# Kernel optimization log

Hardware: AMD Instinct MI355X
Metric: run time of the kernel (lower is better)

## Reference

```python
import jax, jax.numpy as jnp
import numpy as np

H = 8  # num_heads

def setup_inputs() -> dict:
    key = jax.random.key(0)
    k1, k2, k3, k4 = jax.random.split(key, 4)
    B, T, D, K = 16, 8192, 512, 4
    x = jax.random.normal(k1, (B, T, D), dtype=jnp.float32)
    mask = jax.random.randint(k2, (B, T), 0, 2, dtype=jnp.int32)
    queries = jax.random.normal(k3, (1, K, D), dtype=jnp.float32) * 0.02
    # xavier_uniform for (D, D) Linear weight
    limit = np.sqrt(6.0 / (D + D))
    w_out = jax.random.uniform(k4, (D, D), dtype=jnp.float32, minval=-limit, maxval=limit)
    b_out = jnp.zeros((D,), dtype=jnp.float32)
    return {"x": x, "mask": mask, "queries": queries, "w_out": w_out, "b_out": b_out}

def reference(x, mask, queries, w_out, b_out):
    B, T, D = x.shape
    K = queries.shape[1]
    hd = D // H
    scale = jnp.sqrt(jnp.float32(hd))
    q = queries.reshape(K, H, hd)          # shared across batch
    kv = x.reshape(B, T, H, hd)            # keys == values
    scores = jnp.einsum('khd,bthd->bhkt', q, kv) / scale  # (B,H,K,T)
    scores = jnp.where(mask[:, None, None, :] == 0, jnp.float32(-1e9), scores)
    attn = jax.nn.softmax(scores, axis=-1)  # dropout is identity in eval / p=0
    out = jnp.einsum('bhkt,bthd->bkhd', attn, kv).reshape(B, K, D)
    return out @ w_out.T + b_out
```

## Files before the change

### kernel.cpp

```cpp
#include <hip/hip_runtime.h>
#include <math.h>

#define BB 16
#define TT 8192
#define DD 512
#define KK 4
#define HH 8
#define HD 64

__global__ __launch_bounds__(512, 4)
void attn_partial_kernel(const float* __restrict__ x,
                         const int* __restrict__ mask,
                         const float* __restrict__ queries,
                         float* __restrict__ ws,
                         int NC) {
    const int C     = TT / NC;
    const int iters = C >> 3;
    const int b     = blockIdx.x / NC;
    const int c     = blockIdx.x % NC;
    const int t0    = c * C;
    const int tid   = threadIdx.x;
    const int slot  = tid >> 6;
    const int seg   = tid & 63;
    const int h     = seg >> 3;
    const int qd    = seg & 7;

    __shared__ int    smask[512];
    __shared__ float4 smerge[8 * 512];
    __shared__ float  smerge_l[8 * 32];

    for (int i = tid; i < C; i += 512) smask[i] = mask[b * TT + t0 + i];
    __syncthreads();

    const float4* q4 = reinterpret_cast<const float4*>(queries);
    float4 qv[4][2];
    #pragma unroll
    for (int k = 0; k < 4; ++k)
        #pragma unroll
        for (int j = 0; j < 2; ++j) {
            float4 v = q4[k * 128 + seg * 2 + j];
            v.x *= 0.125f; v.y *= 0.125f; v.z *= 0.125f; v.w *= 0.125f;
            qv[k][j] = v;
        }

    float4 av[4][2];
    #pragma unroll
    for (int k = 0; k < 4; ++k)
        #pragma unroll
        for (int j = 0; j < 2; ++j) av[k][j] = make_float4(0.f, 0.f, 0.f, 0.f);
    float l[4] = {0.f, 0.f, 0.f, 0.f};

    const float4* xp = reinterpret_cast<const float4*>(x) +
                       ((size_t)(b * TT + t0 + slot)) * 128 + seg * 2;

    float4 pA0 = xp[0], pA1 = xp[1];
    int    mA  = smask[slot];
    float4 pB0 = xp[1024], pB1 = xp[1025];
    int    mB  = smask[8 + slot];
    xp += 2048;

    for (int i = 0; i < iters; i += 2) {
        {
            const float4 x0 = pA0, x1 = pA1;
            const int    mc = mA;
            if (i + 2 < iters) {
                pA0 = xp[0]; pA1 = xp[1];
                mA  = smask[8 * (i + 2) + slot];
                xp += 1024;
            }
            float s[4];
            #pragma unroll
            for (int k = 0; k < 4; ++k) {
                float a;
                a = qv[k][0].x * x0.x;
                a = fmaf(qv[k][0].y, x0.y, a);
                a = fmaf(qv[k][0].z, x0.z, a);
                a = fmaf(qv[k][0].w, x0.w, a);
                a = fmaf(qv[k][1].x, x1.x, a);
                a = fmaf(qv[k][1].y, x1.y, a);
                a = fmaf(qv[k][1].z, x1.z, a);
                a = fmaf(qv[k][1].w, x1.w, a);
                s[k] = a;
            }
            #pragma unroll
            for (int k = 0; k < 4; ++k) {
                s[k] += __shfl_xor(s[k], 1);
                s[k] += __shfl_xor(s[k], 2);
                s[k] += __shfl_xor(s[k], 4);
            }
            #pragma unroll
            for (int k = 0; k < 4; ++k) {
                const float w = mc ? __expf(s[k]) : 0.f;
                l[k] += w;
                av[k][0].x = fmaf(w, x0.x, av[k][0].x);
                av[k][0].y = fmaf(w, x0.y, av[k][0].y);
                av[k][0].z = fmaf(w, x0.z, av[k][0].z);
                av[k][0].w = fmaf(w, x0.w, av[k][0].w);
                av[k][1].x = fmaf(w, x1.x, av[k][1].x);
                av[k][1].y = fmaf(w, x1.y, av[k][1].y);
                av[k][1].z = fmaf(w, x1.z, av[k][1].z);
                av[k][1].w = fmaf(w, x1.w, av[k][1].w);
            }
        }
        {
            const float4 x0 = pB0, x1 = pB1;
            const int    mc = mB;
            if (i + 3 < iters) {
                pB0 = xp[0]; pB1 = xp[1];
                mB  = smask[8 * (i + 3) + slot];
                xp += 1024;
            }
            float s[4];
            #pragma unroll
            for (int k = 0; k < 4; ++k) {
                float a;
                a = qv[k][0].x * x0.x;
                a = fmaf(qv[k][0].y, x0.y, a);
                a = fmaf(qv[k][0].z, x0.z, a);
                a = fmaf(qv[k][0].w, x0.w, a);
                a = fmaf(qv[k][1].x, x1.x, a);
                a = fmaf(qv[k][1].y, x1.y, a);
                a = fmaf(qv[k][1].z, x1.z, a);
                a = fmaf(qv[k][1].w, x1.w, a);
                s[k] = a;
            }
            #pragma unroll
            for (int k = 0; k < 4; ++k) {
                s[k] += __shfl_xor(s[k], 1);
                s[k] += __shfl_xor(s[k], 2);
                s[k] += __shfl_xor(s[k], 4);
            }
            #pragma unroll
            for (int k = 0; k < 4; ++k) {
                const float w = mc ? __expf(s[k]) : 0.f;
                l[k] += w;
                av[k][0].x = fmaf(w, x0.x, av[k][0].x);
                av[k][0].y = fmaf(w, x0.y, av[k][0].y);
                av[k][0].z = fmaf(w, x0.z, av[k][0].z);
                av[k][0].w = fmaf(w, x0.w, av[k][0].w);
                av[k][1].x = fmaf(w, x1.x, av[k][1].x);
                av[k][1].y = fmaf(w, x1.y, av[k][1].y);
                av[k][1].z = fmaf(w, x1.z, av[k][1].z);
                av[k][1].w = fmaf(w, x1.w, av[k][1].w);
            }
        }
    }

    #pragma unroll
    for (int k = 0; k < 4; ++k)
        #pragma unroll
        for (int j = 0; j < 2; ++j)
            smerge[slot * 512 + (h * 4 + k) * 16 + qd * 2 + j] = av[k][j];
    if (qd == 0) {
        #pragma unroll
        for (int k = 0; k < 4; ++k) smerge_l[slot * 32 + h * 4 + k] = l[k];
    }
    __syncthreads();

    float4* O4 = reinterpret_cast<float4*>(ws);
    const size_t obase = ((size_t)b * NC + c) * 512;
    {
        float4 sacc = smerge[tid];
        #pragma unroll
        for (int s2 = 1; s2 < 8; ++s2) {
            float4 v = smerge[s2 * 512 + tid];
            sacc.x += v.x; sacc.y += v.y; sacc.z += v.z; sacc.w += v.w;
        }
        O4[obase + tid] = sacc;
    }
    if (tid < 32) {
        float sacc = 0.f;
        #pragma unroll
        for (int s2 = 0; s2 < 8; ++s2) sacc += smerge_l[s2 * 32 + tid];
        float* lp = ws + (size_t)BB * NC * HH * KK * 64;
        lp[(((size_t)b * NC + c) * HH + (tid >> 2)) * KK + (tid & 3)] = sacc;
    }
}

__global__ __launch_bounds__(256, 4)
void merge_gemm_kernel(const float* __restrict__ ws,
                       const float* __restrict__ w_out,
                       const float* __restrict__ b_out,
                       float* __restrict__ out,
                       int NC) {
    const int bk  = blockIdx.x;
    const int b   = bk >> 2;
    const int k   = bk & 3;
    const int tid = threadIdx.x;

    __shared__ __align__(16) float row[512];
    __shared__ float linv[8];

    if (tid < 8) {
        const float* lp = ws + (size_t)BB * NC * HH * KK * 64;
        float s = 0.f;
        for (int c = 0; c < NC; ++c)
            s += lp[(((size_t)b * NC + c) * HH + tid) * KK + k];
        linv[tid] = 1.0f / s;
    }
    __syncthreads();

    for (int item = tid; item < 512; item += 256) {
        const int h = item >> 6, d = item & 63;
        float s = 0.f;
        for (int c = 0; c < NC; ++c)
            s += ws[((((size_t)b * NC + c) * HH + h) * KK + k) * 64 + d];
        row[item] = s * linv[h];
    }
    __syncthreads();

    const float4* W4 = reinterpret_cast<const float4*>(w_out);
    const float4* R4 = reinterpret_cast<const float4*>(row);
    float a0 = b_out[tid];
    float a1 = b_out[tid + 256];
    for (int d4 = 0; d4 < 128; ++d4) {
        const float4 r  = R4[d4];
        const float4 wa = W4[(size_t)tid * 128 + d4];
        const float4 wb = W4[((size_t)tid + 256) * 128 + d4];
        a0 = fmaf(r.x, wa.x, fmaf(r.y, wa.y, fmaf(r.z, wa.z, fmaf(r.w, wa.w, a0))));
        a1 = fmaf(r.x, wb.x, fmaf(r.y, wb.y, fmaf(r.z, wb.z, fmaf(r.w, wb.w, a1))));
    }
    out[(size_t)bk * 512 + tid]       = a0;
    out[(size_t)bk * 512 + tid + 256] = a1;
}

extern "C" void kernel_launch(void* const* d_in, const int* in_sizes, int n_in,
                              void* d_out, int out_size, void* d_ws, size_t ws_size,
                              hipStream_t stream) {
    const float* x       = (const float*)d_in[0];
    const int*   mask    = (const int*)d_in[1];
    const float* queries = (const float*)d_in[2];
    const float* w_out   = (const float*)d_in[3];
    const float* b_out   = (const float*)d_in[4];
    float*       out     = (float*)d_out;
    float*       ws      = (float*)d_ws;

    int NC = 32;
    while (NC > 16 && (size_t)BB * NC * HH * KK * 65 * 4 > ws_size) NC >>= 1;

    attn_partial_kernel<<<BB * NC, 512, 0, stream>>>(x, mask, queries, ws, NC);
    merge_gemm_kernel<<<BB * KK, 256, 0, stream>>>(ws, w_out, b_out, out, NC);
}
```

Baseline: 421.2 us.

## Compact unmasked token indices per chunk and stream only active rows

Each block now builds a compacted list of unmasked token indices in shared memory using wave ballots and a prefix sum. The main loop then iterates only over active tokens (padded to a multiple of eight), so the kernel reads fewer rows of x and does fewer FMAs than before, when it processed every token and zeroed the masked ones. The cost is extra barriers and setup per block, gathered loads that are still row-contiguous, and loop trip counts that vary with the mask density of each chunk.

After: 390.4 us. 1.08x faster.

```diff
diff --git a/kernel.cpp b/kernel.cpp
--- a/kernel.cpp
+++ b/kernel.cpp
@@ -15,7 +15,6 @@
                          float* __restrict__ ws,
                          int NC) {
     const int C     = TT / NC;
-    const int iters = C >> 3;
     const int b     = blockIdx.x / NC;
     const int c     = blockIdx.x % NC;
     const int t0    = c * C;
@@ -28,9 +27,33 @@
     __shared__ int    smask[512];
     __shared__ float4 smerge[8 * 512];
     __shared__ float  smerge_l[8 * 32];
+    __shared__ unsigned short cidx[520];
+    __shared__ int    wtot[8], woff[8], s_nit;
 
     for (int i = tid; i < C; i += 512) smask[i] = mask[b * TT + t0 + i];
     __syncthreads();
+
+    {
+        const int wid = tid >> 6, lane = tid & 63;
+        const int entry = wid * 64 + lane;
+        const bool act = (entry < C) && (smask[entry] != 0);
+        unsigned long long bal = __ballot(act);
+        int pfx = __popcll(bal & ((1ull << lane) - 1));
+        if (lane == 0) wtot[wid] = __popcll(bal);
+        __syncthreads();
+        if (tid == 0) {
+            int acc = 0;
+            #pragma unroll
+            for (int i2 = 0; i2 < 8; ++i2) { woff[i2] = acc; acc += wtot[i2]; }
+            const int padded = (acc + 7) & ~7;
+            for (int i2 = acc; i2 < padded; ++i2) cidx[i2] = 0xFFFFu;
+            s_nit = padded >> 3;
+        }
+        __syncthreads();
+        if (act) cidx[woff[wid] + pfx] = (unsigned short)entry;
+        __syncthreads();
+    }
+    const int nit = s_nit;
 
     const float4* q4 = reinterpret_cast<const float4*>(queries);
     float4 qv[4][2];
@@ -50,99 +73,78 @@
         for (int j = 0; j < 2; ++j) av[k][j] = make_float4(0.f, 0.f, 0.f, 0.f);
     float l[4] = {0.f, 0.f, 0.f, 0.f};
 
-    const float4* xp = reinterpret_cast<const float4*>(x) +
-                       ((size_t)(b * TT + t0 + slot)) * 128 + seg * 2;
-
-    float4 pA0 = xp[0], pA1 = xp[1];
-    int    mA  = smask[slot];
-    float4 pB0 = xp[1024], pB1 = xp[1025];
-    int    mB  = smask[8 + slot];
-    xp += 2048;
-
-    for (int i = 0; i < iters; i += 2) {
+    const float4* x4 = reinterpret_cast<const float4*>(x);
+    const size_t  bbase = (size_t)b * TT * 128 + seg * 2;
+
+    auto process = [&](const float4& x0, const float4& x1, bool valid) {
+        float s[4];
+        #pragma unroll
+        for (int k = 0; k < 4; ++k) {
+            float a;
+            a = qv[k][0].x * x0.x;
+            a = fmaf(qv[k][0].y, x0.y, a);
+            a = fmaf(qv[k][0].z, x0.z, a);
+            a = fmaf(qv[k][0].w, x0.w, a);
+            a = fmaf(qv[k][1].x, x1.x, a);
+            a = fmaf(qv[k][1].y, x1.y, a);
+            a = fmaf(qv[k][1].z, x1.z, a);
+            a = fmaf(qv[k][1].w, x1.w, a);
+            s[k] = a;
+        }
+        #pragma unroll
+        for (int k = 0; k < 4; ++k) {
+            s[k] += __shfl_xor(s[k], 1);
+            s[k] += __shfl_xor(s[k], 2);
+            s[k] += __shfl_xor(s[k], 4);
+        }
+        #pragma unroll
+        for (int k = 0; k < 4; ++k) {
+            const float w = valid ? __expf(s[k]) : 0.f;
+            l[k] += w;
+            av[k][0].x = fmaf(w, x0.x, av[k][0].x);
+            av[k][0].y = fmaf(w, x0.y, av[k][0].y);
+            av[k][0].z = fmaf(w, x0.z, av[k][0].z);
+            av[k][0].w = fmaf(w, x0.w, av[k][0].w);
+            av[k][1].x = fmaf(w, x1.x, av[k][1].x);
+            av[k][1].y = fmaf(w, x1.y, av[k][1].y);
+            av[k][1].z = fmaf(w, x1.z, av[k][1].z);
+            av[k][1].w = fmaf(w, x1.w, av[k][1].w);
+        }
+    };
+
+    float4 pA0 = make_float4(0.f,0.f,0.f,0.f), pA1 = pA0, pB0 = pA0, pB1 = pA0;
+    int rA = -1, rB = -1;
+    if (nit > 0) {
+        int r = cidx[slot]; rA = (r == 0xFFFF) ? -1 : r;
+        const float4* p = x4 + bbase + (size_t)(t0 + (rA < 0 ? 0 : rA)) * 128;
+        pA0 = p[0]; pA1 = p[1];
+    }
+    if (nit > 1) {
+        int r = cidx[8 + slot]; rB = (r == 0xFFFF) ? -1 : r;
+        const float4* p = x4 + bbase + (size_t)(t0 + (rB < 0 ? 0 : rB)) * 128;
+        pB0 = p[0]; pB1 = p[1];
+    }
+
+    for (int g = 0; g < nit; g += 2) {
         {
             const float4 x0 = pA0, x1 = pA1;
-            const int    mc = mA;
-            if (i + 2 < iters) {
-                pA0 = xp[0]; pA1 = xp[1];
-                mA  = smask[8 * (i + 2) + slot];
-                xp += 1024;
+            const bool   va = (rA >= 0);
+            if (g + 2 < nit) {
+                int r = cidx[(g + 2) * 8 + slot]; rA = (r == 0xFFFF) ? -1 : r;
+                const float4* p = x4 + bbase + (size_t)(t0 + (rA < 0 ? 0 : rA)) * 128;
+                pA0 = p[0]; pA1 = p[1];
             }
-            float s[4];
-            #pragma unroll
-            for (int k = 0; k < 4; ++k) {
-                float a;
-                a = qv[k][0].x * x0.x;
-                a = fmaf(qv[k][0].y, x0.y, a);
-                a = fmaf(qv[k][0].z, x0.z, a);
-                a = fmaf(qv[k][0].w, x0.w, a);
-                a = fmaf(qv[k][1].x, x1.x, a);
-                a = fmaf(qv[k][1].y, x1.y, a);
-                a = fmaf(qv[k][1].z, x1.z, a);
-                a = fmaf(qv[k][1].w, x1.w, a);
-                s[k] = a;
+            process(x0, x1, va);
+        }
+        if (g + 1 < nit) {
+            const float4 x0 = pB0, x1 = pB1;
+            const bool   vb = (rB >= 0);
+            if (g + 3 < nit) {
+                int r = cidx[(g + 3) * 8 + slot]; rB = (r == 0xFFFF) ? -1 : r;
+                const float4* p = x4 + bbase + (size_t)(t0 + (rB < 0 ? 0 : rB)) * 128;
+                pB0 = p[0]; pB1 = p[1];
             }
-            #pragma unroll
-            for (int k = 0; k < 4; ++k) {
-                s[k] += __shfl_xor(s[k], 1);
-                s[k] += __shfl_xor(s[k], 2);
-                s[k] += __shfl_xor(s[k], 4);
-            }
-            #pragma unroll
-            for (int k = 0; k < 4; ++k) {
-                const float w = mc ? __expf(s[k]) : 0.f;
-                l[k] += w;
-                av[k][0].x = fmaf(w, x0.x, av[k][0].x);
-                av[k][0].y = fmaf(w, x0.y, av[k][0].y);
-                av[k][0].z = fmaf(w, x0.z, av[k][0].z);
-                av[k][0].w = fmaf(w, x0.w, av[k][0].w);
-                av[k][1].x = fmaf(w, x1.x, av[k][1].x);
-                av[k][1].y = fmaf(w, x1.y, av[k][1].y);
-                av[k][1].z = fmaf(w, x1.z, av[k][1].z);
-                av[k][1].w = fmaf(w, x1.w, av[k][1].w);
-            }
-        }
-        {
-            const float4 x0 = pB0, x1 = pB1;
-            const int    mc = mB;
-            if (i + 3 < iters) {
-                pB0 = xp[0]; pB1 = xp[1];
-                mB  = smask[8 * (i + 3) + slot];
-                xp += 1024;
-            }
-            float s[4];
-            #pragma unroll
-            for (int k = 0; k < 4; ++k) {
-                float a;
-                a = qv[k][0].x * x0.x;
-                a = fmaf(qv[k][0].y, x0.y, a);
-                a = fmaf(qv[k][0].z, x0.z, a);
-                a = fmaf(qv[k][0].w, x0.w, a);
-                a = fmaf(qv[k][1].x, x1.x, a);
-                a = fmaf(qv[k][1].y, x1.y, a);
-                a = fmaf(qv[k][1].z, x1.z, a);
-                a = fmaf(qv[k][1].w, x1.w, a);
-                s[k] = a;
-            }
-            #pragma unroll
-            for (int k = 0; k < 4; ++k) {
-                s[k] += __shfl_xor(s[k], 1);
-                s[k] += __shfl_xor(s[k], 2);
-                s[k] += __shfl_xor(s[k], 4);
-            }
-            #pragma unroll
-            for (int k = 0; k < 4; ++k) {
-                const float w = mc ? __expf(s[k]) : 0.f;
-                l[k] += w;
-                av[k][0].x = fmaf(w, x0.x, av[k][0].x);
-                av[k][0].y = fmaf(w, x0.y, av[k][0].y);
-                av[k][0].z = fmaf(w, x0.z, av[k][0].z);
-                av[k][0].w = fmaf(w, x0.w, av[k][0].w);
-                av[k][1].x = fmaf(w, x1.x, av[k][1].x);
-                av[k][1].y = fmaf(w, x1.y, av[k][1].y);
-                av[k][1].z = fmaf(w, x1.z, av[k][1].z);
-                av[k][1].w = fmaf(w, x1.w, av[k][1].w);
-            }
+            process(x0, x1, vb);
         }
     }
 
```
